# Kernel tuning notes

Measured on AMD Instinct MI355X. Metric: run time of the kernel, lower is better.

## Reference

```python
import jax, jax.numpy as jnp
import numpy as np

MASK_CHANNEL = 0
STEPS = 8          # = fill_max of t; loop iterations beyond each sample's t are masked no-ops
D_SCALE = 0.2      # diffusion coefficient scale (stability over STEPS explicit-Euler steps)
RHO_SCALE = 0.1    # reaction rate scale


def _laplacian(u):
    # 5-point periodic stencil on [B, H, W]
    return (jnp.roll(u, 1, -1) + jnp.roll(u, -1, -1)
            + jnp.roll(u, 1, -2) + jnp.roll(u, -1, -2) - 4.0 * u)


def setup_inputs() -> dict:
    key = jax.random.key(0)
    k1, k2, k3 = jax.random.split(key, 3)
    x = jax.random.uniform(k1, (32, 4, 512, 512), dtype=jnp.float32)
    t = jax.random.randint(k2, (32,), 0, STEPS).astype(jnp.int32)
    W = (jax.random.normal(k3, (4, 2), dtype=jnp.float32) * 0.1)
    b = jnp.zeros((2,), jnp.float32)
    return {"x": x, "W": W, "b": b, "t": t}


def reference(x, W, b, t):
    # Equivalent of PDEEval.forward: per step i, select samples with t > i,
    # compute per-sample PDE params, apply one explicit-Euler PDE update to the
    # mask channel, scatter-add back. Boolean select + scatter is expressed as a
    # masked dense update (identical math, jit-friendly static shapes).
    def step(xc, i):
        mask = (t > i)                                   # [B]
        feats = xc.mean(axis=(2, 3))                     # [B, C] global pool (params provider)
        p = jax.nn.sigmoid(feats @ W + b)                # [B, 2]
        D = p[:, 0] * D_SCALE                            # [B]
        rho = p[:, 1] * RHO_SCALE                        # [B]
        u = xc[:, MASK_CHANNEL]                          # [B, H, W] tumor density field
        diff = D[:, None, None] * _laplacian(u) + rho[:, None, None] * u * (1.0 - u)
        upd = jnp.zeros_like(xc).at[:, MASK_CHANNEL].set(diff)
        xc = xc + jnp.where(mask[:, None, None, None], upd, 0.0)
        return xc, None

    x, _ = jax.lax.scan(step, x, jnp.arange(STEPS))
    return x
```

## Files before the change

kernel.cpp:

```cpp
#include <hip/hip_runtime.h>
#include <cstddef>

#define NB 32
#define NC 4
#define NH 512
#define NW 512
#define PLANE (NH * NW)
#define NSTEPS 8
#define SROWS 8
#define NSTRIP (NH / SROWS)

typedef float v4f __attribute__((ext_vector_type(4)));

__device__ __forceinline__ float blockReduce256(float v, float* sm) {
#pragma unroll
    for (int off = 32; off > 0; off >>= 1) v += __shfl_down(v, off, 64);
    int lane = threadIdx.x & 63;
    int wave = threadIdx.x >> 6;
    if (lane == 0) sm[wave] = v;
    __syncthreads();
    return (threadIdx.x == 0) ? ((sm[0] + sm[1]) + (sm[2] + sm[3])) : 0.0f;
}

__global__ void mean_copy_kernel(const float* __restrict__ x,
                                 float* __restrict__ out,
                                 float* __restrict__ sumsAll,
                                 float* __restrict__ stepSums,
                                 const int* __restrict__ tg) {
    int id = blockIdx.x;
    int sub = id & 15;
    int plane = id >> 4;
    int c = plane & 3;
    int b = plane >> 4 >> 0;
    b = plane >> 2;
    size_t base = (size_t)plane * PLANE + (size_t)sub * (PLANE / 16);
    const v4f* s4 = (const v4f*)(x + base);
    v4f* d4 = (v4f*)(out + base);
    const int nvec = PLANE / 16 / 4;
    float s = 0.0f;
    if (c == 0) {
        bool doStore = (tg[b] == 0);
        for (int j = threadIdx.x; j < nvec; j += 256) {
            v4f v = s4[j];
            s += (v.x + v.y) + (v.z + v.w);
            if (doStore) __builtin_nontemporal_store(v, &d4[j]);
        }
    } else {
        for (int j = threadIdx.x; j < nvec; j += 256) {
            v4f v = __builtin_nontemporal_load(&s4[j]);
            s += (v.x + v.y) + (v.z + v.w);
            __builtin_nontemporal_store(v, &d4[j]);
        }
    }
    __shared__ float sm[4];
    float tot = blockReduce256(s, sm);
    if (threadIdx.x == 0) {
        if (c == 0) atomicAdd(&stepSums[b], tot);
        else atomicAdd(&sumsAll[b * NC + c], tot);
    }
}

__global__ __launch_bounds__(256) void step_kernel(
    const float* __restrict__ x, float* __restrict__ out, float* __restrict__ ws,
    const float* __restrict__ sumsAll, const float* __restrict__ stepSums,
    const float* __restrict__ Wm, const float* __restrict__ bv,
    const int* __restrict__ tg, int stepIdx) {
    __shared__ int tSh[NB];
    __shared__ float prm[2];
    __shared__ float sm[4];
    if (threadIdx.x < NB) tSh[threadIdx.x] = tg[threadIdx.x];
    __syncthreads();

    int item = blockIdx.y;
    int b = -1, tb = 0, cnt = 0;
#pragma unroll
    for (int bb = 0; bb < NB; ++bb) {
        int tv = tSh[bb];
        if (tv > stepIdx) {
            if (cnt == item) { b = bb; tb = tv; }
            ++cnt;
        }
    }
    if (b < 0) return;

    if (threadIdx.x == 0) {
        const float inv = 1.0f / (float)PLANE;
        float f0 = stepSums[stepIdx * NB + b] * inv;
        float f1 = sumsAll[b * NC + 1] * inv;
        float f2 = sumsAll[b * NC + 2] * inv;
        float f3 = sumsAll[b * NC + 3] * inv;
        float z0 = f0 * Wm[0] + f1 * Wm[2] + f2 * Wm[4] + f3 * Wm[6] + bv[0];
        float z1 = f0 * Wm[1] + f1 * Wm[3] + f2 * Wm[5] + f3 * Wm[7] + bv[1];
        prm[0] = 0.2f / (1.0f + expf(-z0));
        prm[1] = 0.1f / (1.0f + expf(-z1));
    }
    __syncthreads();
    float D = prm[0], rho = prm[1];

    const float* sp = (stepIdx == 0) ? (x + (size_t)b * NC * PLANE)
                    : (stepIdx & 1)  ? (ws + (size_t)b * PLANE)
                                     : (out + (size_t)b * NC * PLANE);
    bool finalStep = (stepIdx == tb - 1);
    float* dp = (finalStep || (stepIdx & 1)) ? (out + (size_t)b * NC * PLANE)
                                             : (ws + (size_t)b * PLANE);

    int col4 = threadIdx.x & 127;
    int x0 = col4 * 4;
    int half = threadIdx.x >> 7;
    int lane = threadIdx.x & 63;
    int y0 = blockIdx.x * SROWS + half * (SROWS / 2);

    v4f up = ((const v4f*)(sp + (size_t)((y0 - 1) & (NH - 1)) * NW))[col4];
    v4f cc = ((const v4f*)(sp + (size_t)y0 * NW))[col4];
    float acc = 0.0f;
#pragma unroll
    for (int k = 0; k < SROWS / 2; ++k) {
        int y = y0 + k;
        v4f dn = ((const v4f*)(sp + (size_t)((y + 1) & (NH - 1)) * NW))[col4];
        float lft = __shfl_up(cc.w, 1, 64);
        if (lane == 0) lft = sp[(size_t)y * NW + ((x0 - 1) & (NW - 1))];
        float rgt = __shfl_down(cc.x, 1, 64);
        if (lane == 63) rgt = sp[(size_t)y * NW + ((x0 + 4) & (NW - 1))];
        v4f un;
        un.x = cc.x + (D * (up.x + dn.x + lft + cc.y - 4.0f * cc.x) + rho * cc.x * (1.0f - cc.x));
        un.y = cc.y + (D * (up.y + dn.y + cc.x + cc.z - 4.0f * cc.y) + rho * cc.y * (1.0f - cc.y));
        un.z = cc.z + (D * (up.z + dn.z + cc.y + cc.w - 4.0f * cc.z) + rho * cc.z * (1.0f - cc.z));
        un.w = cc.w + (D * (up.w + dn.w + cc.z + rgt - 4.0f * cc.w) + rho * cc.w * (1.0f - cc.w));
        if (finalStep) __builtin_nontemporal_store(un, &((v4f*)(dp + (size_t)y * NW))[col4]);
        else ((v4f*)(dp + (size_t)y * NW))[col4] = un;
        acc += (un.x + un.y) + (un.z + un.w);
        up = cc; cc = dn;
    }

    if (stepIdx + 1 < tb) {
        float tot = blockReduce256(acc, sm);
        if (threadIdx.x == 0) atomicAdd((float*)&stepSums[(stepIdx + 1) * NB + b], tot);
    }
}

extern "C" void kernel_launch(void* const* d_in, const int* in_sizes, int n_in,
                              void* d_out, int out_size, void* d_ws, size_t ws_size,
                              hipStream_t stream) {
    const float* x = (const float*)d_in[0];
    const float* Wm = (const float*)d_in[1];
    const float* bv = (const float*)d_in[2];
    const int* t = (const int*)d_in[3];
    float* out = (float*)d_out;

    float* wsU = (float*)d_ws;
    float* sumsAll = wsU + (size_t)NB * PLANE;
    float* stepSums = sumsAll + NB * NC;

    hipMemsetAsync(sumsAll, 0, sizeof(float) * (NB * NC + NSTEPS * NB), stream);

    mean_copy_kernel<<<NB * NC * 16, 256, 0, stream>>>(x, out, sumsAll, stepSums, t);

    for (int i = 0; i < NSTEPS - 1; ++i) {
        dim3 grid(NSTRIP, NB);
        step_kernel<<<grid, 256, 0, stream>>>(x, out, wsU, sumsAll, stepSums,
                                              Wm, bv, t, i);
    }
}
```

Measured before the change: 345.9 us.

## Fuse mean-copy and all PDE steps into one persistent kernel with per-sample barriers

Replaces the initial copy/mean kernel and the seven per-step launches with a single kernel of 1024 blocks, 32 per sample. Blocks synchronise through global atomic barriers per sample, and each block writes its partial sums to slots that are reduced deterministically instead of with atomicAdd. This removes launch gaps and the idle blocks launched for inactive samples, and it keeps each block's strip cache-resident across steps. The barriers spin and depend on all 1024 blocks being co-resident, so the kernel can deadlock if occupancy is lower than the launch bound assumes.

```diff
diff --git a/kernel.cpp b/kernel.cpp
--- a/kernel.cpp
+++ b/kernel.cpp
@@ -7,8 +7,9 @@
 #define NW 512
 #define PLANE (NH * NW)
 #define NSTEPS 8
-#define SROWS 8
-#define NSTRIP (NH / SROWS)
+#define GBLK 32
+#define SROWS (NH / GBLK)
+#define NBLOCKS (NB * GBLK)
 
 typedef float v4f __attribute__((ext_vector_type(4)));
 
@@ -19,122 +20,152 @@
     int wave = threadIdx.x >> 6;
     if (lane == 0) sm[wave] = v;
     __syncthreads();
-    return (threadIdx.x == 0) ? ((sm[0] + sm[1]) + (sm[2] + sm[3])) : 0.0f;
+    float r = (threadIdx.x == 0) ? ((sm[0] + sm[1]) + (sm[2] + sm[3])) : 0.0f;
+    __syncthreads();
+    return r;
 }
 
-__global__ void mean_copy_kernel(const float* __restrict__ x,
-                                 float* __restrict__ out,
-                                 float* __restrict__ sumsAll,
-                                 float* __restrict__ stepSums,
-                                 const int* __restrict__ tg) {
-    int id = blockIdx.x;
-    int sub = id & 15;
-    int plane = id >> 4;
-    int c = plane & 3;
-    int b = plane >> 4 >> 0;
-    b = plane >> 2;
-    size_t base = (size_t)plane * PLANE + (size_t)sub * (PLANE / 16);
-    const v4f* s4 = (const v4f*)(x + base);
-    v4f* d4 = (v4f*)(out + base);
-    const int nvec = PLANE / 16 / 4;
-    float s = 0.0f;
-    if (c == 0) {
-        bool doStore = (tg[b] == 0);
-        for (int j = threadIdx.x; j < nvec; j += 256) {
-            v4f v = s4[j];
-            s += (v.x + v.y) + (v.z + v.w);
-            if (doStore) __builtin_nontemporal_store(v, &d4[j]);
+__device__ __forceinline__ void groupBarrier(unsigned* bar, int tgt) {
+    __syncthreads();
+    __threadfence();
+    if (threadIdx.x == 0) {
+        __hip_atomic_fetch_add(bar, 1u, __ATOMIC_ACQ_REL, __HIP_MEMORY_SCOPE_AGENT);
+        while (__hip_atomic_load(bar, __ATOMIC_ACQUIRE, __HIP_MEMORY_SCOPE_AGENT) <
+               (unsigned)tgt)
+            __builtin_amdgcn_s_sleep(2);
+    }
+    __syncthreads();
+    __threadfence();
+}
+
+__global__ __launch_bounds__(256, 4) void fused_kernel(
+    const float* __restrict__ x, float* __restrict__ out, float* __restrict__ ws,
+    float* __restrict__ partA,
+    float* __restrict__ stepPart,
+    unsigned* __restrict__ bar,
+    const float* __restrict__ Wm, const float* __restrict__ bv,
+    const int* __restrict__ tg) {
+    __shared__ float sm[4];
+    __shared__ float prm[2];
+    int b = blockIdx.x >> 5;
+    int s = blockIdx.x & 31;
+    int tb = tg[b];
+
+    const size_t xb = (size_t)b * NC * PLANE;
+    const int rows0 = s * SROWS;
+    const int nvec = SROWS * NW / 4;
+
+    {
+        const v4f* s4 = (const v4f*)(x + xb + (size_t)rows0 * NW);
+        v4f* d4 = (v4f*)(out + xb + (size_t)rows0 * NW);
+        float a0 = 0.0f;
+        if (tb == 0) {
+            for (int j = threadIdx.x; j < nvec; j += 256) {
+                v4f v = s4[j];
+                a0 += (v.x + v.y) + (v.z + v.w);
+                __builtin_nontemporal_store(v, &d4[j]);
+            }
+        } else {
+            for (int j = threadIdx.x; j < nvec; j += 256) {
+                v4f v = s4[j];
+                a0 += (v.x + v.y) + (v.z + v.w);
+            }
         }
-    } else {
-        for (int j = threadIdx.x; j < nvec; j += 256) {
-            v4f v = __builtin_nontemporal_load(&s4[j]);
-            s += (v.x + v.y) + (v.z + v.w);
-            __builtin_nontemporal_store(v, &d4[j]);
+        float a123[3];
+#pragma unroll
+        for (int c = 1; c < 4; ++c) {
+            const v4f* sc = (const v4f*)(x + xb + (size_t)c * PLANE + (size_t)rows0 * NW);
+            v4f* dc = (v4f*)(out + xb + (size_t)c * PLANE + (size_t)rows0 * NW);
+            float a = 0.0f;
+            for (int j = threadIdx.x; j < nvec; j += 256) {
+                v4f v = __builtin_nontemporal_load(&sc[j]);
+                a += (v.x + v.y) + (v.z + v.w);
+                __builtin_nontemporal_store(v, &dc[j]);
+            }
+            a123[c - 1] = a;
+        }
+        float t0 = blockReduce256(a0, sm);
+        float t1 = blockReduce256(a123[0], sm);
+        float t2 = blockReduce256(a123[1], sm);
+        float t3 = blockReduce256(a123[2], sm);
+        if (threadIdx.x == 0) {
+            stepPart[b * GBLK + s] = t0;
+            partA[(b * 3 + 0) * GBLK + s] = t1;
+            partA[(b * 3 + 1) * GBLK + s] = t2;
+            partA[(b * 3 + 2) * GBLK + s] = t3;
         }
     }
-    __shared__ float sm[4];
-    float tot = blockReduce256(s, sm);
-    if (threadIdx.x == 0) {
-        if (c == 0) atomicAdd(&stepSums[b], tot);
-        else atomicAdd(&sumsAll[b * NC + c], tot);
-    }
-}
+    if (tb == 0) return;
 
-__global__ __launch_bounds__(256) void step_kernel(
-    const float* __restrict__ x, float* __restrict__ out, float* __restrict__ ws,
-    const float* __restrict__ sumsAll, const float* __restrict__ stepSums,
-    const float* __restrict__ Wm, const float* __restrict__ bv,
-    const int* __restrict__ tg, int stepIdx) {
-    __shared__ int tSh[NB];
-    __shared__ float prm[2];
-    __shared__ float sm[4];
-    if (threadIdx.x < NB) tSh[threadIdx.x] = tg[threadIdx.x];
-    __syncthreads();
+    int syncs = 1;
+    groupBarrier(&bar[b], GBLK * syncs);
 
-    int item = blockIdx.y;
-    int b = -1, tb = 0, cnt = 0;
+    for (int i = 0; i < tb; ++i) {
+        if (threadIdx.x < 64) {
+            int l = threadIdx.x & 31;
+            float f0 = stepPart[(i * NB + b) * GBLK + l];
+            float f1 = partA[(b * 3 + 0) * GBLK + l];
+            float f2 = partA[(b * 3 + 1) * GBLK + l];
+            float f3 = partA[(b * 3 + 2) * GBLK + l];
 #pragma unroll
-    for (int bb = 0; bb < NB; ++bb) {
-        int tv = tSh[bb];
-        if (tv > stepIdx) {
-            if (cnt == item) { b = bb; tb = tv; }
-            ++cnt;
+            for (int off = 16; off > 0; off >>= 1) {
+                f0 += __shfl_down(f0, off, 32);
+                f1 += __shfl_down(f1, off, 32);
+                f2 += __shfl_down(f2, off, 32);
+                f3 += __shfl_down(f3, off, 32);
+            }
+            if (threadIdx.x == 0) {
+                const float inv = 1.0f / (float)PLANE;
+                f0 *= inv; f1 *= inv; f2 *= inv; f3 *= inv;
+                float z0 = f0 * Wm[0] + f1 * Wm[2] + f2 * Wm[4] + f3 * Wm[6] + bv[0];
+                float z1 = f0 * Wm[1] + f1 * Wm[3] + f2 * Wm[5] + f3 * Wm[7] + bv[1];
+                prm[0] = 0.2f / (1.0f + expf(-z0));
+                prm[1] = 0.1f / (1.0f + expf(-z1));
+            }
         }
-    }
-    if (b < 0) return;
+        __syncthreads();
+        float D = prm[0], rho = prm[1];
 
-    if (threadIdx.x == 0) {
-        const float inv = 1.0f / (float)PLANE;
-        float f0 = stepSums[stepIdx * NB + b] * inv;
-        float f1 = sumsAll[b * NC + 1] * inv;
-        float f2 = sumsAll[b * NC + 2] * inv;
-        float f3 = sumsAll[b * NC + 3] * inv;
-        float z0 = f0 * Wm[0] + f1 * Wm[2] + f2 * Wm[4] + f3 * Wm[6] + bv[0];
-        float z1 = f0 * Wm[1] + f1 * Wm[3] + f2 * Wm[5] + f3 * Wm[7] + bv[1];
-        prm[0] = 0.2f / (1.0f + expf(-z0));
-        prm[1] = 0.1f / (1.0f + expf(-z1));
-    }
-    __syncthreads();
-    float D = prm[0], rho = prm[1];
+        const float* sp = (i == 0) ? (x + xb)
+                        : (i & 1)  ? (ws + (size_t)b * PLANE)
+                                   : (out + xb);
+        bool fin = (i == tb - 1);
+        float* dp = (fin || (i & 1)) ? (out + xb) : (ws + (size_t)b * PLANE);
 
-    const float* sp = (stepIdx == 0) ? (x + (size_t)b * NC * PLANE)
-                    : (stepIdx & 1)  ? (ws + (size_t)b * PLANE)
-                                     : (out + (size_t)b * NC * PLANE);
-    bool finalStep = (stepIdx == tb - 1);
-    float* dp = (finalStep || (stepIdx & 1)) ? (out + (size_t)b * NC * PLANE)
-                                             : (ws + (size_t)b * PLANE);
+        int col4 = threadIdx.x & 127;
+        int x0 = col4 * 4;
+        int half = threadIdx.x >> 7;
+        int lane = threadIdx.x & 63;
+        int y0 = rows0 + half * (SROWS / 2);
 
-    int col4 = threadIdx.x & 127;
-    int x0 = col4 * 4;
-    int half = threadIdx.x >> 7;
-    int lane = threadIdx.x & 63;
-    int y0 = blockIdx.x * SROWS + half * (SROWS / 2);
+        v4f up = ((const v4f*)(sp + (size_t)((y0 - 1) & (NH - 1)) * NW))[col4];
+        v4f cc = ((const v4f*)(sp + (size_t)y0 * NW))[col4];
+        float acc = 0.0f;
+#pragma unroll
+        for (int k = 0; k < SROWS / 2; ++k) {
+            int y = y0 + k;
+            v4f dn = ((const v4f*)(sp + (size_t)((y + 1) & (NH - 1)) * NW))[col4];
+            float lft = __shfl_up(cc.w, 1, 64);
+            if (lane == 0) lft = sp[(size_t)y * NW + ((x0 - 1) & (NW - 1))];
+            float rgt = __shfl_down(cc.x, 1, 64);
+            if (lane == 63) rgt = sp[(size_t)y * NW + ((x0 + 4) & (NW - 1))];
+            v4f un;
+            un.x = cc.x + (D * (up.x + dn.x + lft + cc.y - 4.0f * cc.x) + rho * cc.x * (1.0f - cc.x));
+            un.y = cc.y + (D * (up.y + dn.y + cc.x + cc.z - 4.0f * cc.y) + rho * cc.y * (1.0f - cc.y));
+            un.z = cc.z + (D * (up.z + dn.z + cc.y + cc.w - 4.0f * cc.z) + rho * cc.z * (1.0f - cc.z));
+            un.w = cc.w + (D * (up.w + dn.w + cc.z + rgt - 4.0f * cc.w) + rho * cc.w * (1.0f - cc.w));
+            if (fin) __builtin_nontemporal_store(un, &((v4f*)(dp + (size_t)y * NW))[col4]);
+            else ((v4f*)(dp + (size_t)y * NW))[col4] = un;
+            acc += (un.x + un.y) + (un.z + un.w);
+            up = cc; cc = dn;
+        }
 
-    v4f up = ((const v4f*)(sp + (size_t)((y0 - 1) & (NH - 1)) * NW))[col4];
-    v4f cc = ((const v4f*)(sp + (size_t)y0 * NW))[col4];
-    float acc = 0.0f;
-#pragma unroll
-    for (int k = 0; k < SROWS / 2; ++k) {
-        int y = y0 + k;
-        v4f dn = ((const v4f*)(sp + (size_t)((y + 1) & (NH - 1)) * NW))[col4];
-        float lft = __shfl_up(cc.w, 1, 64);
-        if (lane == 0) lft = sp[(size_t)y * NW + ((x0 - 1) & (NW - 1))];
-        float rgt = __shfl_down(cc.x, 1, 64);
-        if (lane == 63) rgt = sp[(size_t)y * NW + ((x0 + 4) & (NW - 1))];
-        v4f un;
-        un.x = cc.x + (D * (up.x + dn.x + lft + cc.y - 4.0f * cc.x) + rho * cc.x * (1.0f - cc.x));
-        un.y = cc.y + (D * (up.y + dn.y + cc.x + cc.z - 4.0f * cc.y) + rho * cc.y * (1.0f - cc.y));
-        un.z = cc.z + (D * (up.z + dn.z + cc.y + cc.w - 4.0f * cc.z) + rho * cc.z * (1.0f - cc.z));
-        un.w = cc.w + (D * (up.w + dn.w + cc.z + rgt - 4.0f * cc.w) + rho * cc.w * (1.0f - cc.w));
-        if (finalStep) __builtin_nontemporal_store(un, &((v4f*)(dp + (size_t)y * NW))[col4]);
-        else ((v4f*)(dp + (size_t)y * NW))[col4] = un;
-        acc += (un.x + un.y) + (un.z + un.w);
-        up = cc; cc = dn;
-    }
-
-    if (stepIdx + 1 < tb) {
-        float tot = blockReduce256(acc, sm);
-        if (threadIdx.x == 0) atomicAdd((float*)&stepSums[(stepIdx + 1) * NB + b], tot);
+        if (!fin) {
+            float tot = blockReduce256(acc, sm);
+            if (threadIdx.x == 0) stepPart[((i + 1) * NB + b) * GBLK + s] = tot;
+            ++syncs;
+            groupBarrier(&bar[b], GBLK * syncs);
+        }
     }
 }
 
@@ -148,16 +179,12 @@
     float* out = (float*)d_out;
 
     float* wsU = (float*)d_ws;
-    float* sumsAll = wsU + (size_t)NB * PLANE;
-    float* stepSums = sumsAll + NB * NC;
+    float* partA = wsU + (size_t)NB * PLANE;
+    float* stepPart = partA + NB * 3 * GBLK;
+    unsigned* bar = (unsigned*)(stepPart + NSTEPS * NB * GBLK);
 
-    hipMemsetAsync(sumsAll, 0, sizeof(float) * (NB * NC + NSTEPS * NB), stream);
+    hipMemsetAsync(bar, 0, sizeof(unsigned) * NB, stream);
 
-    mean_copy_kernel<<<NB * NC * 16, 256, 0, stream>>>(x, out, sumsAll, stepSums, t);
-
-    for (int i = 0; i < NSTEPS - 1; ++i) {
-        dim3 grid(NSTRIP, NB);
-        step_kernel<<<grid, 256, 0, stream>>>(x, out, wsU, sumsAll, stepSums,
-                                              Wm, bv, t, i);
-    }
+    fused_kernel<<<NBLOCKS, 256, 0, stream>>>(x, out, wsU, partA, stepPart, bar,
+                                              Wm, bv, t);
 }
```

After: 1.262 ms. 3.65x slower.
